# Kernel optimization log

Hardware: AMD Instinct MI355X
Metric: run time of the kernel (lower is better)

The kernel has to match this reference:

```python
import jax, jax.numpy as jnp
import numpy as np

N = 100_000      # nodes
E = 1_600_000    # directed edges
D_IN, D_H, D_OUT = 128, 128, 1


def setup_inputs() -> dict:
    key = jax.random.key(0)
    ks = jax.random.split(key, 6)
    x = jax.random.normal(ks[0], (N, D_IN), dtype=jnp.float32)
    edge_index = jax.random.randint(ks[1], (2, E), 0, N, dtype=jnp.int32)
    # GCNConv params (glorot-ish scale)
    W1 = jax.random.normal(ks[2], (D_IN, D_H), dtype=jnp.float32) / np.sqrt(D_IN)
    b1 = jnp.zeros((D_H,), dtype=jnp.float32)
    W2 = jax.random.normal(ks[3], (D_H, D_OUT), dtype=jnp.float32) / np.sqrt(D_H)
    b2 = jnp.zeros((D_OUT,), dtype=jnp.float32)
    return {"x": x, "edge_index": edge_index, "W1": W1, "b1": b1, "W2": W2, "b2": b2}


def _gcn_layer(x, src, dst, norm, W, b):
    # PyG GCNConv: linear transform, then sym-normalized neighbor sum (self-loops included in src/dst)
    h = x @ W                                  # [N, d_out]
    msg = h[src] * norm[:, None]               # [E+N, d_out] gather + scale
    out = jax.ops.segment_sum(msg, dst, num_segments=N)  # scatter-add
    return out + b


def reference(x, edge_index, W1, b1, W2, b2):
    loops = jnp.arange(N, dtype=edge_index.dtype)
    src = jnp.concatenate([edge_index[0], loops])  # [E+N]
    dst = jnp.concatenate([edge_index[1], loops])
    # symmetric normalization D^{-1/2} (A+I) D^{-1/2}
    deg = jax.ops.segment_sum(jnp.ones_like(dst, dtype=x.dtype), dst, num_segments=N)
    dis = jnp.where(deg > 0, jax.lax.rsqrt(deg), 0.0)
    norm = dis[src] * dis[dst]
    h = jax.nn.relu(_gcn_layer(x, src, dst, norm, W1, b1))
    return _gcn_layer(h, src, dst, norm, W2, b2)
```

## Files before the change

### kernel.cpp

```cpp
#include <hip/hip_runtime.h>
#include <hip/hip_fp16.h>

#define D 128
#define BSHIFT 9
#define MAXB 512
#define CHUNK 8192
#define CAP 12288
#define GP 8

typedef _Float16 f16x8 __attribute__((ext_vector_type(8)));
typedef float f32x4 __attribute__((ext_vector_type(4)));

__global__ void setup_k(const float* __restrict__ W1, _Float16* __restrict__ w1t,
                        int* __restrict__ bcur) {
    int idx = blockIdx.x * 256 + threadIdx.x;
    int k = idx >> 7, n = idx & 127;
    w1t[n * 128 + k] = (_Float16)W1[idx];
    if (blockIdx.x == 0) {
        bcur[threadIdx.x] = 0;
        bcur[threadIdx.x + 256] = 0;
    }
}

__global__ __launch_bounds__(512) void bin_k(const int* __restrict__ src,
                                             const int* __restrict__ dst,
                                             int* __restrict__ bcur,
                                             unsigned int* __restrict__ pairs, int E) {
    __shared__ int h[MAXB];
    __shared__ int cur[MAXB];
    if (threadIdx.x < MAXB) h[threadIdx.x] = 0;
    __syncthreads();
    const int base = blockIdx.x * CHUNK;
    int s_[16], d_[16];
    int n = 0;
#pragma unroll
    for (int u = 0; u < 16; ++u) {
        int e = base + u * 512 + threadIdx.x;
        if (e < E) {
            s_[u] = src[e];
            d_[u] = dst[e];
            atomicAdd(&h[d_[u] >> BSHIFT], 1);
            n = u + 1;
        }
    }
    __syncthreads();
    if (threadIdx.x < MAXB) {
        int i = threadIdx.x;
        cur[i] = h[i] ? (i * CAP + atomicAdd(&bcur[i], h[i])) : 0;
    }
    __syncthreads();
#pragma unroll
    for (int u = 0; u < 16; ++u) {
        if (u < n) {
            int b = d_[u] >> BSHIFT;
            int pos = atomicAdd(&cur[b], 1);
            if (pos - b * CAP < CAP)
                pairs[pos] = ((unsigned int)(d_[u] & ((1 << BSHIFT) - 1)) << 23) |
                             (unsigned int)s_[u];
        }
    }
}

__global__ __launch_bounds__(512) void csr_k(const unsigned int* __restrict__ pairs,
                                             const int* __restrict__ bcur,
                                             int* __restrict__ offs,
                                             int* __restrict__ deg,
                                             float* __restrict__ dis,
                                             int* __restrict__ edge_src, int N) {
    __shared__ int hist[512];
    __shared__ int scan[512];
    __shared__ int cur[512];
    const int b = blockIdx.x;
    const int t = threadIdx.x;
    const int vb = b << BSHIFT;
    const int ebeg = b * CAP;
    int cnt = bcur[b]; cnt = cnt < CAP ? cnt : CAP;
    const int eend = ebeg + cnt;

    hist[t] = 0;
    __syncthreads();
    for (int e = ebeg + t; e < eend; e += 512)
        atomicAdd(&hist[pairs[e] >> 23], 1);
    __syncthreads();

    const int c = hist[t];
    const int p4 = (c + 3) & ~3;
    scan[t] = p4;
    __syncthreads();
    for (int o = 1; o < 512; o <<= 1) {
        int a = (t >= o) ? scan[t - o] : 0;
        __syncthreads();
        scan[t] += a;
        __syncthreads();
    }

    {
        int v = vb + t;
        if (v < N) {
            int base = ebeg + scan[t] - p4;
            offs[v] = base;
            deg[v] = c;
            cur[t] = base;
            dis[v] = rsqrtf((float)(c + 1));
        }
    }
    __syncthreads();

    for (int e = ebeg + t; e < eend; e += 512) {
        unsigned int p = pairs[e];
        int pos = atomicAdd(&cur[p >> 23], 1);
        edge_src[pos] = (int)(p & 0x7FFFFFu);
    }
}


__global__ __launch_bounds__(256) void gemm_k(const float* __restrict__ x,
                                              const _Float16* __restrict__ w1t,
                                              const float* __restrict__ dis,
                                              __half2* __restrict__ h1s2, int N) {
    __shared__ _Float16 xs[128][128 + GP];
    __shared__ _Float16 ws[128][128 + GP];

    const int tid = threadIdx.x;
    const int row0 = blockIdx.x * 128;

#pragma unroll
    for (int u = 0; u < 16; ++u) {
        int f = u * 256 + tid;
        int r = f >> 5, c4 = f & 31;
        int rg = row0 + r; rg = rg < N ? rg : N - 1;
        float4 v = ((const float4*)(x + (size_t)rg * D))[c4];
        union { _Float16 h[4]; uint2 u2; } tmp;
        tmp.h[0] = (_Float16)v.x; tmp.h[1] = (_Float16)v.y;
        tmp.h[2] = (_Float16)v.z; tmp.h[3] = (_Float16)v.w;
        *(uint2*)&xs[r][c4 * 4] = tmp.u2;
    }
#pragma unroll
    for (int u = 0; u < 8; ++u) {
        int f = u * 256 + tid;
        int r = f >> 4, c8 = f & 15;
        int4 v = ((const int4*)(w1t + r * 128))[c8];
        *(int4*)&ws[r][c8 * 8] = v;
    }
    __syncthreads();

    const int wave = tid >> 6, lane = tid & 63;
    const int qr = lane & 15;
    const int quad = lane >> 4;
    const int m0 = wave * 32;

    f32x4 acc[2][8] = {};
#pragma unroll
    for (int kt = 0; kt < 4; ++kt) {
        const int kk = kt * 32 + quad * 8;
        f16x8 a0 = *(const f16x8*)&xs[m0 + qr][kk];
        f16x8 a1 = *(const f16x8*)&xs[m0 + 16 + qr][kk];
#pragma unroll
        for (int n = 0; n < 8; ++n) {
            f16x8 b = *(const f16x8*)&ws[n * 16 + qr][kk];
            acc[0][n] = __builtin_amdgcn_mfma_f32_16x16x32_f16(a0, b, acc[0][n], 0, 0, 0);
            acc[1][n] = __builtin_amdgcn_mfma_f32_16x16x32_f16(a1, b, acc[1][n], 0, 0, 0);
        }
    }

    float dv[2][4];
#pragma unroll
    for (int mt = 0; mt < 2; ++mt)
#pragma unroll
        for (int r = 0; r < 4; ++r) {
            int rg = row0 + m0 + mt * 16 + quad * 4 + r;
            dv[mt][r] = dis[rg < N ? rg : 0];
        }

    __syncthreads();
#pragma unroll
    for (int mt = 0; mt < 2; ++mt)
#pragma unroll
        for (int n = 0; n < 8; ++n)
#pragma unroll
            for (int r = 0; r < 4; ++r)
                xs[m0 + mt * 16 + quad * 4 + r][n * 16 + qr] =
                    (_Float16)(acc[mt][n][r] * dv[mt][r]);
    __syncthreads();

#pragma unroll
    for (int u = 0; u < 8; ++u) {
        int f = u * 256 + tid;
        int r = f >> 4, c8 = f & 15;
        int rg = row0 + r;
        if (rg < N)
            *(int4*)((_Float16*)h1s2 + (size_t)rg * D + c8 * 8) = *(int4*)&xs[r][c8 * 8];
    }
}


__global__ __launch_bounds__(256) void agg1_k(const __half2* __restrict__ h1s2,
                                              const int* __restrict__ edge_src,
                                              const int* __restrict__ offs,
                                              const int* __restrict__ deg,
                                              const float* __restrict__ dis,
                                              const float* __restrict__ b1,
                                              const float* __restrict__ W2,
                                              float* __restrict__ g, int N) {
    const int c = threadIdx.x & 15;
    const int v = blockIdx.x * 16 + (threadIdx.x >> 4);
    if (v >= N) return;
    const _Float16* __restrict__ h1 = (const _Float16*)h1s2;

    float a[8];
    {
        f16x8 hv = *(const f16x8*)(h1 + (size_t)v * 128 + c * 8);
#pragma unroll
        for (int k = 0; k < 8; ++k) a[k] = (float)hv[k];
    }

    const int beg = offs[v];
    const int rem = deg[v];
    const int* ep = edge_src + beg;

    for (int i = 0; i < rem; i += 8) {
        int4 s0 = *(const int4*)(ep + i);
        int4 s1 = {};
        if (i + 4 < rem) s1 = *(const int4*)(ep + i + 4);
        f16x8 r0 = {}, r1 = {}, r2 = {}, r3 = {}, r4 = {}, r5 = {}, r6 = {}, r7 = {};
        r0 = *(const f16x8*)(h1 + (size_t)s0.x * 128 + c * 8);
        if (i + 1 < rem) r1 = *(const f16x8*)(h1 + (size_t)s0.y * 128 + c * 8);
        if (i + 2 < rem) r2 = *(const f16x8*)(h1 + (size_t)s0.z * 128 + c * 8);
        if (i + 3 < rem) r3 = *(const f16x8*)(h1 + (size_t)s0.w * 128 + c * 8);
        if (i + 4 < rem) r4 = *(const f16x8*)(h1 + (size_t)s1.x * 128 + c * 8);
        if (i + 5 < rem) r5 = *(const f16x8*)(h1 + (size_t)s1.y * 128 + c * 8);
        if (i + 6 < rem) r6 = *(const f16x8*)(h1 + (size_t)s1.z * 128 + c * 8);
        if (i + 7 < rem) r7 = *(const f16x8*)(h1 + (size_t)s1.w * 128 + c * 8);
#pragma unroll
        for (int k = 0; k < 8; ++k)
            a[k] += (((float)r0[k] + (float)r1[k]) + ((float)r2[k] + (float)r3[k]))
                  + (((float)r4[k] + (float)r5[k]) + ((float)r6[k] + (float)r7[k]));
    }

    const float dv = dis[v];
    const float4 ba = ((const float4*)b1)[c * 2];
    const float4 bb = ((const float4*)b1)[c * 2 + 1];
    const float4 wa = ((const float4*)W2)[c * 2];
    const float4 wb = ((const float4*)W2)[c * 2 + 1];
    float p = fmaxf(fmaf(dv, a[0], ba.x), 0.f) * wa.x
            + fmaxf(fmaf(dv, a[1], ba.y), 0.f) * wa.y
            + fmaxf(fmaf(dv, a[2], ba.z), 0.f) * wa.z
            + fmaxf(fmaf(dv, a[3], ba.w), 0.f) * wa.w
            + fmaxf(fmaf(dv, a[4], bb.x), 0.f) * wb.x
            + fmaxf(fmaf(dv, a[5], bb.y), 0.f) * wb.y
            + fmaxf(fmaf(dv, a[6], bb.z), 0.f) * wb.z
            + fmaxf(fmaf(dv, a[7], bb.w), 0.f) * wb.w;
#pragma unroll
    for (int o = 8; o >= 1; o >>= 1) p += __shfl_xor(p, o, 64);
    if (c == 0) g[v] = dv * p;
}


__global__ void agg2_k(const float* __restrict__ g, const int* __restrict__ edge_src,
                       const int* __restrict__ offs, const int* __restrict__ deg,
                       const float* __restrict__ dis, const float* __restrict__ b2,
                       float* __restrict__ out, int N) {
    int v = blockIdx.x * 256 + threadIdx.x;
    if (v >= N) return;
    float acc = g[v];
    const int beg = offs[v];
    const int d = deg[v];
    int i = 0;
    for (; i + 4 <= d; i += 4) {
        int4 s = *(const int4*)&edge_src[beg + i];
        acc += (g[s.x] + g[s.y]) + (g[s.z] + g[s.w]);
    }
    for (; i < d; ++i) acc += g[edge_src[beg + i]];
    out[v] = fmaf(dis[v], acc, b2[0]);
}


extern "C" void kernel_launch(void* const* d_in, const int* in_sizes, int n_in,
                              void* d_out, int out_size, void* d_ws, size_t ws_size,
                              hipStream_t stream) {
    const float* x  = (const float*)d_in[0];
    const int*   ei = (const int*)d_in[1];
    const float* W1 = (const float*)d_in[2];
    const float* b1 = (const float*)d_in[3];
    const float* W2 = (const float*)d_in[4];
    const float* b2 = (const float*)d_in[5];
    float* out = (float*)d_out;

    const int N = in_sizes[0] / D;
    const int E = in_sizes[1] / 2;
    const int* srcp = ei;
    const int* dstp = ei + E;
    const int nbuck = (N + (1 << BSHIFT) - 1) >> BSHIFT;

    char* p = (char*)d_ws;
    auto alloc = [&](size_t bytes) {
        void* q = (void*)p;
        p += (bytes + 255) & ~(size_t)255;
        return q;
    };
    __half2*      h1s2     = (__half2*)alloc((size_t)N * D * sizeof(__half));
    float*        g        = (float*)alloc((size_t)N * sizeof(float));
    float*        dis      = (float*)alloc((size_t)N * sizeof(float));
    int*          offs     = (int*)alloc((size_t)N * sizeof(int));
    int*          deg      = (int*)alloc((size_t)N * sizeof(int));
    int*          edge_src = (int*)alloc((size_t)nbuck * CAP * sizeof(int));
    unsigned int* pairs    = (unsigned int*)alloc((size_t)nbuck * CAP * sizeof(unsigned int));
    _Float16*     w1t      = (_Float16*)alloc((size_t)D * D * sizeof(_Float16));
    int*          bcur     = (int*)alloc(MAXB * sizeof(int));

    const int nb = (N + 255) / 256;

    setup_k<<<(D * D) / 256, 256, 0, stream>>>(W1, w1t, bcur);
    bin_k<<<(E + CHUNK - 1) / CHUNK, 512, 0, stream>>>(srcp, dstp, bcur, pairs, E);
    csr_k<<<nbuck, 512, 0, stream>>>(pairs, bcur, offs, deg, dis, edge_src, N);
    gemm_k<<<(N + 127) / 128, 256, 0, stream>>>(x, w1t, dis, h1s2, N);
    agg1_k<<<(N + 15) / 16, 256, 0, stream>>>(h1s2, edge_src, offs, deg, dis, b1, W2, g, N);
    agg2_k<<<nb, 256, 0, stream>>>(g, edge_src, offs, deg, dis, b2, out, N);
}
```

Measured before the change: 202.9 us.

## Pad CSR rows to multiples of eight with zero sentinel node, branchless gathers

```diff
diff --git a/kernel.cpp b/kernel.cpp
--- a/kernel.cpp
+++ b/kernel.cpp
@@ -12,13 +12,19 @@
 typedef float f32x4 __attribute__((ext_vector_type(4)));
 
 __global__ void setup_k(const float* __restrict__ W1, _Float16* __restrict__ w1t,
-                        int* __restrict__ bcur) {
+                        int* __restrict__ bcur, __half2* __restrict__ h1s2,
+                        float* __restrict__ g, int N) {
     int idx = blockIdx.x * 256 + threadIdx.x;
     int k = idx >> 7, n = idx & 127;
     w1t[n * 128 + k] = (_Float16)W1[idx];
     if (blockIdx.x == 0) {
         bcur[threadIdx.x] = 0;
         bcur[threadIdx.x + 256] = 0;
+        if (threadIdx.x < 16) {
+            int4 z = {0, 0, 0, 0};
+            ((int4*)(h1s2 + (size_t)N * 64))[threadIdx.x] = z;
+        }
+        if (threadIdx.x == 0) g[N] = 0.f;
     }
 }
 
@@ -70,6 +76,7 @@
     __shared__ int hist[512];
     __shared__ int scan[512];
     __shared__ int cur[512];
+    __shared__ int buf[CAP];
     const int b = blockIdx.x;
     const int t = threadIdx.x;
     const int vb = b << BSHIFT;
@@ -78,14 +85,15 @@
     const int eend = ebeg + cnt;
 
     hist[t] = 0;
+    for (int j = t; j < CAP; j += 512) buf[j] = N;
     __syncthreads();
     for (int e = ebeg + t; e < eend; e += 512)
         atomicAdd(&hist[pairs[e] >> 23], 1);
     __syncthreads();
 
     const int c = hist[t];
-    const int p4 = (c + 3) & ~3;
-    scan[t] = p4;
+    const int p8 = (c + 7) & ~7;
+    scan[t] = p8;
     __syncthreads();
     for (int o = 1; o < 512; o <<= 1) {
         int a = (t >= o) ? scan[t - o] : 0;
@@ -93,14 +101,15 @@
         scan[t] += a;
         __syncthreads();
     }
+    const int total = scan[511];
 
     {
         int v = vb + t;
         if (v < N) {
-            int base = ebeg + scan[t] - p4;
-            offs[v] = base;
+            int base_rel = scan[t] - p8;
+            offs[v] = ebeg + base_rel;
             deg[v] = c;
-            cur[t] = base;
+            cur[t] = base_rel;
             dis[v] = rsqrtf((float)(c + 1));
         }
     }
@@ -109,8 +118,13 @@
     for (int e = ebeg + t; e < eend; e += 512) {
         unsigned int p = pairs[e];
         int pos = atomicAdd(&cur[p >> 23], 1);
-        edge_src[pos] = (int)(p & 0x7FFFFFu);
-    }
+        buf[pos] = (int)(p & 0x7FFFFFu);
+    }
+    __syncthreads();
+
+    const int n4 = total >> 2;
+    for (int j = t; j < n4; j += 512)
+        ((int4*)(edge_src + ebeg))[j] = ((const int4*)buf)[j];
 }
 
 
@@ -194,14 +208,14 @@
 }
 
 
-__global__ __launch_bounds__(256) void agg1_k(const __half2* __restrict__ h1s2,
-                                              const int* __restrict__ edge_src,
-                                              const int* __restrict__ offs,
-                                              const int* __restrict__ deg,
-                                              const float* __restrict__ dis,
-                                              const float* __restrict__ b1,
-                                              const float* __restrict__ W2,
-                                              float* __restrict__ g, int N) {
+__global__ __launch_bounds__(256, 6) void agg1_k(const __half2* __restrict__ h1s2,
+                                                 const int* __restrict__ edge_src,
+                                                 const int* __restrict__ offs,
+                                                 const int* __restrict__ deg,
+                                                 const float* __restrict__ dis,
+                                                 const float* __restrict__ b1,
+                                                 const float* __restrict__ W2,
+                                                 float* __restrict__ g, int N) {
     const int c = threadIdx.x & 15;
     const int v = blockIdx.x * 16 + (threadIdx.x >> 4);
     if (v >= N) return;
@@ -209,32 +223,32 @@
 
     float a[8];
     {
-        f16x8 hv = *(const f16x8*)(h1 + (size_t)v * 128 + c * 8);
+        f16x8 hv = *(const f16x8*)(h1 + v * 128 + c * 8);
 #pragma unroll
         for (int k = 0; k < 8; ++k) a[k] = (float)hv[k];
     }
 
     const int beg = offs[v];
-    const int rem = deg[v];
-    const int* ep = edge_src + beg;
-
-    for (int i = 0; i < rem; i += 8) {
-        int4 s0 = *(const int4*)(ep + i);
-        int4 s1 = {};
-        if (i + 4 < rem) s1 = *(const int4*)(ep + i + 4);
-        f16x8 r0 = {}, r1 = {}, r2 = {}, r3 = {}, r4 = {}, r5 = {}, r6 = {}, r7 = {};
-        r0 = *(const f16x8*)(h1 + (size_t)s0.x * 128 + c * 8);
-        if (i + 1 < rem) r1 = *(const f16x8*)(h1 + (size_t)s0.y * 128 + c * 8);
-        if (i + 2 < rem) r2 = *(const f16x8*)(h1 + (size_t)s0.z * 128 + c * 8);
-        if (i + 3 < rem) r3 = *(const f16x8*)(h1 + (size_t)s0.w * 128 + c * 8);
-        if (i + 4 < rem) r4 = *(const f16x8*)(h1 + (size_t)s1.x * 128 + c * 8);
-        if (i + 5 < rem) r5 = *(const f16x8*)(h1 + (size_t)s1.y * 128 + c * 8);
-        if (i + 6 < rem) r6 = *(const f16x8*)(h1 + (size_t)s1.z * 128 + c * 8);
-        if (i + 7 < rem) r7 = *(const f16x8*)(h1 + (size_t)s1.w * 128 + c * 8);
-#pragma unroll
-        for (int k = 0; k < 8; ++k)
-            a[k] += (((float)r0[k] + (float)r1[k]) + ((float)r2[k] + (float)r3[k]))
-                  + (((float)r4[k] + (float)r5[k]) + ((float)r6[k] + (float)r7[k]));
+    const int p8 = (deg[v] + 7) & ~7;
+    const int4* ip = (const int4*)(edge_src + beg);
+    int4 s0 = ip[0], s1 = ip[1];
+
+    for (int i = 0; i < p8; i += 8) {
+        int4 n0 = ip[2], n1 = ip[3];
+        f16x8 r0 = *(const f16x8*)(h1 + s0.x * 128 + c * 8);
+        f16x8 r1 = *(const f16x8*)(h1 + s0.y * 128 + c * 8);
+        f16x8 r2 = *(const f16x8*)(h1 + s0.z * 128 + c * 8);
+        f16x8 r3 = *(const f16x8*)(h1 + s0.w * 128 + c * 8);
+        f16x8 r4 = *(const f16x8*)(h1 + s1.x * 128 + c * 8);
+        f16x8 r5 = *(const f16x8*)(h1 + s1.y * 128 + c * 8);
+        f16x8 r6 = *(const f16x8*)(h1 + s1.z * 128 + c * 8);
+        f16x8 r7 = *(const f16x8*)(h1 + s1.w * 128 + c * 8);
+        f16x8 t0 = r0 + r1, t1 = r2 + r3, t2 = r4 + r5, t3 = r6 + r7;
+        f16x8 u0 = t0 + t1, u1 = t2 + t3;
+        f16x8 w = u0 + u1;
+#pragma unroll
+        for (int k = 0; k < 8; ++k) a[k] += (float)w[k];
+        s0 = n0; s1 = n1; ip += 2;
     }
 
     const float dv = dis[v];
@@ -264,13 +278,12 @@
     if (v >= N) return;
     float acc = g[v];
     const int beg = offs[v];
-    const int d = deg[v];
-    int i = 0;
-    for (; i + 4 <= d; i += 4) {
-        int4 s = *(const int4*)&edge_src[beg + i];
+    const int p8 = (deg[v] + 7) & ~7;
+    const int4* ip = (const int4*)(edge_src + beg);
+    for (int i = 0; i < p8; i += 4) {
+        int4 s = ip[i >> 2];
         acc += (g[s.x] + g[s.y]) + (g[s.z] + g[s.w]);
     }
-    for (; i < d; ++i) acc += g[edge_src[beg + i]];
     out[v] = fmaf(dis[v], acc, b2[0]);
 }
 
@@ -298,8 +311,8 @@
         p += (bytes + 255) & ~(size_t)255;
         return q;
     };
-    __half2*      h1s2     = (__half2*)alloc((size_t)N * D * sizeof(__half));
-    float*        g        = (float*)alloc((size_t)N * sizeof(float));
+    __half2*      h1s2     = (__half2*)alloc((size_t)(N + 1) * D * sizeof(__half));
+    float*        g        = (float*)alloc((size_t)(N + 1) * sizeof(float));
     float*        dis      = (float*)alloc((size_t)N * sizeof(float));
     int*          offs     = (int*)alloc((size_t)N * sizeof(int));
     int*          deg      = (int*)alloc((size_t)N * sizeof(int));
@@ -310,7 +323,7 @@
 
     const int nb = (N + 255) / 256;
 
-    setup_k<<<(D * D) / 256, 256, 0, stream>>>(W1, w1t, bcur);
+    setup_k<<<(D * D) / 256, 256, 0, stream>>>(W1, w1t, bcur, h1s2, g, N);
     bin_k<<<(E + CHUNK - 1) / CHUNK, 512, 0, stream>>>(srcp, dstp, bcur, pairs, E);
     csr_k<<<nbuck, 512, 0, stream>>>(pairs, bcur, offs, deg, dis, edge_src, N);
     gemm_k<<<(N + 127) / 128, 256, 0, stream>>>(x, w1t, dis, h1s2, N);
```

New measurement: 201.0 us. Within noise of the previous version (-1.0%).
